# Kernel optimization log

Measured on AMD Instinct MI355X. Metric: run time of the kernel, lower is better.

The kernel has to match this reference:

```python
import jax, jax.numpy as jnp
import numpy as np

DIM = 1024
HEADS = 16
DIM_HEAD = DIM // HEADS

def setup_inputs() -> dict:
    key = jax.random.key(0)
    k1, k2, k3 = jax.random.split(key, 3)
    x = jax.random.normal(k1, (2, 2048, DIM), dtype=jnp.float32)
    # nn.Linear(dim, 3*dim, bias=False): weight [3*dim, dim]; y = x @ W.T
    W_qkv = jax.random.normal(k2, (3 * DIM, DIM), dtype=jnp.float32) * (1.0 / np.sqrt(DIM))
    W_out = jax.random.normal(k3, (DIM, DIM), dtype=jnp.float32) * (1.0 / np.sqrt(DIM))
    return {"x": x, "W_qkv": W_qkv, "W_out": W_out}

def reference(x, W_qkv, W_out):
    b, s, _ = x.shape
    scale = DIM_HEAD ** -0.5
    qkv = x @ W_qkv.T                              # [b, s, 3*dim]
    q, k, v = jnp.split(qkv, 3, axis=-1)
    def to_heads(t):
        return t.reshape(b, s, HEADS, DIM_HEAD).transpose(0, 2, 1, 3)  # [b,h,s,d]
    q, k, v = map(to_heads, (q, k, v))
    scores = jnp.einsum('bhid,bhjd->bhij', q, k) * scale
    causal_mask = jnp.triu(jnp.ones((s, s), dtype=bool), k=1)
    scores = jnp.where(causal_mask, -jnp.inf, scores)
    attn = jax.nn.softmax(scores, axis=-1)
    out = jnp.einsum('bhij,bhjd->bhid', attn, v)
    out = out.transpose(0, 2, 1, 3).reshape(b, s, HEADS * DIM_HEAD)
    return out @ W_out.T
```

## Files before the change

### kernel.cpp

```cpp
#include <hip/hip_runtime.h>
#include <hip/hip_bf16.h>
#include <math.h>

using bf16 = __hip_bfloat16;
typedef __attribute__((ext_vector_type(8))) short bf16x8;
typedef __attribute__((ext_vector_type(4))) short bf16x4;
typedef __attribute__((ext_vector_type(4))) float f32x4;
typedef __attribute__((ext_vector_type(2))) int i32x2;

static __device__ __forceinline__ void gl_lds16(const void* g, void* l) {
  __builtin_amdgcn_global_load_lds(
      (const __attribute__((address_space(1))) unsigned int*)g,
      (__attribute__((address_space(3))) unsigned int*)l, 16, 0, 0);
}

#define MFMA16 __builtin_amdgcn_mfma_f32_16x16x32_bf16
#define MFMA16K16 __builtin_amdgcn_mfma_f32_16x16x16bf16_1k

static __device__ __forceinline__ short f2bf(float f) {
  return (short)((__builtin_bit_cast(unsigned int, f) + 0x8000u) >> 16);
}

__global__ __launch_bounds__(256) void cvt_all(
    const float* __restrict__ x, const float* __restrict__ wqkv,
    const float* __restrict__ wout, bf16* __restrict__ xb,
    bf16* __restrict__ wqkvb, bf16* __restrict__ woutb) {
  const int blk = blockIdx.x;
  const float* src;
  bf16* dst;
  int base;
  if (blk < 4096) {
    src = x; dst = xb; base = blk;
  } else if (blk < 7168) {
    src = wqkv; dst = wqkvb; base = blk - 4096;
  } else {
    src = wout; dst = woutb; base = blk - 7168;
  }
  const int i = (base * 256 + threadIdx.x) * 4;
  const float4 v = *(const float4*)(src + i);
  bf16x4 o;
  o.x = f2bf(v.x);
  o.y = f2bf(v.y);
  o.z = f2bf(v.z);
  o.w = f2bf(v.w);
  *(bf16x4*)(dst + i) = o;
}

template <int K>
static __device__ __forceinline__ void gemm_bt_acc(
    const bf16* __restrict__ A, const bf16* __restrict__ B,
    int rowA0, int rowB0, bf16* As, bf16* Bs, f32x4 acc[4][4]) {
  const int t = threadIdx.x;
  const int w = t >> 6, l = t & 63;
  const int quad = l >> 4, l16 = l & 15;
  const int wm = (w >> 1) * 64, wn = (w & 1) * 64;
  const int c0 = t, c1 = t + 256;
  const bf16* a0 = A + (size_t)(rowA0 + (c0 >> 2)) * K + (c0 & 3) * 8;
  const bf16* a1 = A + (size_t)(rowA0 + (c1 >> 2)) * K + (c1 & 3) * 8;
  const bf16* b0 = B + (size_t)(rowB0 + (c0 >> 2)) * K + (c0 & 3) * 8;
  const bf16* b1 = B + (size_t)(rowB0 + (c1 >> 2)) * K + (c1 & 3) * 8;
  for (int k0 = 0; k0 < K; k0 += 32) {
    __syncthreads();
    gl_lds16(a0 + k0, As + c0 * 8);
    gl_lds16(a1 + k0, As + c1 * 8);
    gl_lds16(b0 + k0, Bs + c0 * 8);
    gl_lds16(b1 + k0, Bs + c1 * 8);
    __syncthreads();
    bf16x8 af[4], bg[4];
#pragma unroll
    for (int i = 0; i < 4; i++)
      af[i] = *(const bf16x8*)(As + (wm + i * 16 + l16) * 32 + quad * 8);
#pragma unroll
    for (int j = 0; j < 4; j++)
      bg[j] = *(const bf16x8*)(Bs + (wn + j * 16 + l16) * 32 + quad * 8);
#pragma unroll
    for (int i = 0; i < 4; i++)
#pragma unroll
      for (int j = 0; j < 4; j++)
        acc[i][j] = MFMA16(af[i], bg[j], acc[i][j], 0, 0, 0);
  }
}

__global__ __launch_bounds__(256) void qkv_gemm(
    const bf16* __restrict__ x, const bf16* __restrict__ Wqkv,
    bf16* __restrict__ Qb, bf16* __restrict__ Kb, bf16* __restrict__ Vt) {
  __shared__ bf16 As[128 * 32];
  __shared__ bf16 Bs[128 * 32];
  f32x4 acc[4][4];
#pragma unroll
  for (int i = 0; i < 4; i++)
#pragma unroll
    for (int j = 0; j < 4; j++) acc[i][j] = (f32x4){0.f, 0.f, 0.f, 0.f};
  const int bm = blockIdx.x, bn = blockIdx.y;
  gemm_bt_acc<1024>(x, Wqkv, bm * 128, bn * 128, As, Bs, acc);

  const int t = threadIdx.x, w = t >> 6, l = t & 63;
  const int quad = l >> 4, l16 = l & 15;
  const int wm = (w >> 1) * 64, wn = (w & 1) * 64;
#pragma unroll
  for (int i = 0; i < 4; i++) {
    const int m0 = bm * 128 + wm + i * 16 + quad * 4;
    const int b = m0 >> 11, s0 = m0 & 2047;
#pragma unroll
    for (int j = 0; j < 4; j++) {
      const int n = bn * 128 + wn + j * 16 + l16;
      const int which = n >> 10;
      const int nn = n & 1023;
      const int h = nn >> 6, d = nn & 63;
      const int bh = b * 16 + h;
      if (which == 2) {
        bf16x4 v4;
#pragma unroll
        for (int r = 0; r < 4; r++)
          v4[r] = (short)__builtin_bit_cast(unsigned short,
                                            __float2bfloat16(acc[i][j][r]));
        *(bf16x4*)(Vt + ((size_t)bh * 64 + d) * 2048 + s0) = v4;
      } else {
        const float sc = (which == 0) ? 0.125f : 1.0f;
        bf16* dst = (which == 0) ? Qb : Kb;
#pragma unroll
        for (int r = 0; r < 4; r++)
          dst[((size_t)bh * 2048 + s0 + r) * 64 + d] =
              __float2bfloat16(acc[i][j][r] * sc);
      }
    }
  }
}

__global__ __launch_bounds__(256) void attn_kernel(
    const bf16* __restrict__ Qb, const bf16* __restrict__ Kb,
    const bf16* __restrict__ Vt, bf16* __restrict__ attn) {
  __shared__ bf16 Qs[64 * 64];
  __shared__ bf16 Ks[128 * 64];
  __shared__ bf16 Vts[64 * 128];
  const int x = blockIdx.x;
  const int bh = x & 31;
  const int idx = x >> 5;
  const int t = threadIdx.x, w = t >> 6, l = t & 63;
  const int quad = l >> 4, l16 = l & 15;
  const bf16x4 ones = {16256, 16256, 16256, 16256};
  const int b = bh >> 4, h = bh & 15;

  for (int pass = 0; pass < 2; pass++) {
    const int qt = pass ? 31 - idx : idx;
    const int q0 = qt * 64;
    if (pass) __syncthreads();

    const bf16* Qg = Qb + ((size_t)bh * 2048 + q0) * 64;
#pragma unroll
    for (int c = t; c < 512; c += 256) {
      const int row = c >> 3, pos = c & 7;
      gl_lds16(Qg + (row * 8 + (pos ^ (row & 7))) * 8, Qs + c * 8);
    }

    f32x4 oacc[4];
    f32x4 lacc = (f32x4){0.f, 0.f, 0.f, 0.f};
#pragma unroll
    for (int md = 0; md < 4; md++) oacc[md] = (f32x4){0.f, 0.f, 0.f, 0.f};

    const int njj = (qt + 2) >> 1;
    for (int jj = 0; jj < njj; jj++) {
      const int j0 = jj * 128;
      __syncthreads();
      const bf16* Kg = Kb + ((size_t)bh * 2048 + j0) * 64;
#pragma unroll
      for (int c = t; c < 1024; c += 256) {
        const int row = c >> 3, pos = c & 7;
        gl_lds16(Kg + (row * 8 + (pos ^ (row & 7))) * 8, Ks + c * 8);
      }
      const bf16* Vg = Vt + (size_t)bh * 64 * 2048 + j0;
#pragma unroll
      for (int c = t; c < 1024; c += 256) {
        const int d = c >> 4, pos = c & 15;
        gl_lds16(Vg + (size_t)d * 2048 + ((pos ^ (d & 15)) * 8), Vts + c * 8);
      }
      __syncthreads();

      f32x4 sacc[8];
#pragma unroll
      for (int mt = 0; mt < 8; mt++) sacc[mt] = (f32x4){0.f, 0.f, 0.f, 0.f};
#pragma unroll
      for (int kk = 0; kk < 2; kk++) {
        const int qrow = w * 16 + l16;
        const int qpos = (kk * 4 + quad) ^ (qrow & 7);
        bf16x8 qf = *(const bf16x8*)(Qs + qrow * 64 + qpos * 8);
#pragma unroll
        for (int mt = 0; mt < 8; mt++) {
          const int row = mt * 16 + l16;
          const int pos = (kk * 4 + quad) ^ (row & 7);
          bf16x8 kf = *(const bf16x8*)(Ks + row * 64 + pos * 8);
          sacc[mt] = MFMA16(kf, qf, sacc[mt], 0, 0, 0);
        }
      }

      bf16x4 pfrag[8];
      if (jj == njj - 1) {
        const int qi = q0 + w * 16 + l16;
#pragma unroll
        for (int mt = 0; mt < 8; mt++) {
          unsigned rb[4];
#pragma unroll
          for (int r = 0; r < 4; r++) {
            const int sg = j0 + mt * 16 + quad * 4 + r;
            const float p = (sg <= qi) ? __expf(sacc[mt][r]) : 0.f;
            rb[r] = __builtin_bit_cast(unsigned, p) + 0x8000u;
          }
          i32x2 pk;
          pk.x = (int)__builtin_amdgcn_perm(rb[1], rb[0], 0x07060302u);
          pk.y = (int)__builtin_amdgcn_perm(rb[3], rb[2], 0x07060302u);
          pfrag[mt] = __builtin_bit_cast(bf16x4, pk);
        }
      } else {
#pragma unroll
        for (int mt = 0; mt < 8; mt++) {
          unsigned rb[4];
#pragma unroll
          for (int r = 0; r < 4; r++) {
            const float p = __expf(sacc[mt][r]);
            rb[r] = __builtin_bit_cast(unsigned, p) + 0x8000u;
          }
          i32x2 pk;
          pk.x = (int)__builtin_amdgcn_perm(rb[1], rb[0], 0x07060302u);
          pk.y = (int)__builtin_amdgcn_perm(rb[3], rb[2], 0x07060302u);
          pfrag[mt] = __builtin_bit_cast(bf16x4, pk);
        }
      }

#pragma unroll
      for (int kt = 0; kt < 8; kt++) {
        lacc = MFMA16K16(ones, pfrag[kt], lacc, 0, 0, 0);
#pragma unroll
        for (int md = 0; md < 4; md++) {
          const int d = md * 16 + l16;
          const int pos = (kt * 2 + (quad >> 1)) ^ (d & 15);
          bf16x4 va =
              *(const bf16x4*)(Vts + d * 128 + pos * 8 + (quad & 1) * 4);
          oacc[md] = MFMA16K16(va, pfrag[kt], oacc[md], 0, 0, 0);
        }
      }
    }

    const float inv = 1.0f / lacc[0];
    const int srow = q0 + w * 16 + l16;
#pragma unroll
    for (int md = 0; md < 4; md++) {
      bf16x4 o4;
#pragma unroll
      for (int r = 0; r < 4; r++) o4[r] = f2bf(oacc[md][r] * inv);
      *(bf16x4*)(attn + ((size_t)b * 2048 + srow) * 1024 + h * 64 + md * 16 +
                 quad * 4) = o4;
    }
  }
}

__global__ __launch_bounds__(256) void out_gemm(
    const bf16* __restrict__ attn, const bf16* __restrict__ Wout,
    float* __restrict__ out) {
  __shared__ bf16 As[128 * 32];
  __shared__ bf16 Bs[64 * 32];
  f32x4 acc[4][2];
#pragma unroll
  for (int i = 0; i < 4; i++)
#pragma unroll
    for (int j = 0; j < 2; j++) acc[i][j] = (f32x4){0.f, 0.f, 0.f, 0.f};
  const int bm = blockIdx.x, bn = blockIdx.y;
  const int t = threadIdx.x, w = t >> 6, l = t & 63;
  const int quad = l >> 4, l16 = l & 15;
  const int wm = (w >> 1) * 64, wn = (w & 1) * 32;
  const int c0 = t, c1 = t + 256;
  const bf16* a0 = attn + (size_t)(bm * 128 + (c0 >> 2)) * 1024 + (c0 & 3) * 8;
  const bf16* a1 = attn + (size_t)(bm * 128 + (c1 >> 2)) * 1024 + (c1 & 3) * 8;
  const bf16* b0 = Wout + (size_t)(bn * 64 + (t >> 2)) * 1024 + (t & 3) * 8;
  for (int k0 = 0; k0 < 1024; k0 += 32) {
    __syncthreads();
    gl_lds16(a0 + k0, As + c0 * 8);
    gl_lds16(a1 + k0, As + c1 * 8);
    gl_lds16(b0 + k0, Bs + t * 8);
    __syncthreads();
    bf16x8 af[4], bg[2];
#pragma unroll
    for (int i = 0; i < 4; i++)
      af[i] = *(const bf16x8*)(As + (wm + i * 16 + l16) * 32 + quad * 8);
#pragma unroll
    for (int j = 0; j < 2; j++)
      bg[j] = *(const bf16x8*)(Bs + (wn + j * 16 + l16) * 32 + quad * 8);
#pragma unroll
    for (int i = 0; i < 4; i++)
#pragma unroll
      for (int j = 0; j < 2; j++)
        acc[i][j] = MFMA16(af[i], bg[j], acc[i][j], 0, 0, 0);
  }
#pragma unroll
  for (int i = 0; i < 4; i++) {
#pragma unroll
    for (int j = 0; j < 2; j++) {
      const int n = bn * 64 + wn + j * 16 + l16;
#pragma unroll
      for (int r = 0; r < 4; r++) {
        const int m = bm * 128 + wm + i * 16 + quad * 4 + r;
        out[(size_t)m * 1024 + n] = acc[i][j][r];
      }
    }
  }
}

extern "C" void kernel_launch(void* const* d_in, const int* in_sizes, int n_in,
                              void* d_out, int out_size, void* d_ws, size_t ws_size,
                              hipStream_t stream) {
  const float* x = (const float*)d_in[0];
  const float* Wqkv = (const float*)d_in[1];
  const float* Wout = (const float*)d_in[2];
  float* out = (float*)d_out;

  char* ws = (char*)d_ws;
  const size_t MB = 1024 * 1024;
  bf16* xb = (bf16*)(ws + 0 * MB);
  bf16* at = (bf16*)(ws + 0 * MB);
  bf16* Wqkvb = (bf16*)(ws + 8 * MB);
  bf16* Woutb = (bf16*)(ws + 14 * MB);
  bf16* Qb = (bf16*)(ws + 16 * MB);
  bf16* Kb = (bf16*)(ws + 24 * MB);
  bf16* Vt = (bf16*)(ws + 32 * MB);

  cvt_all<<<8192, 256, 0, stream>>>(x, Wqkv, Wout, xb, Wqkvb, Woutb);
  qkv_gemm<<<dim3(32, 24), 256, 0, stream>>>(xb, Wqkvb, Qb, Kb, Vt);
  attn_kernel<<<512, 256, 0, stream>>>(Qb, Kb, Vt, at);
  out_gemm<<<dim3(32, 16), 256, 0, stream>>>(at, Woutb, out);
}
```

Before: 166.2 us.

## Double-buffer K/V tiles in attention with async prefetch and MFMA priority

```diff
diff --git a/kernel.cpp b/kernel.cpp
--- a/kernel.cpp
+++ b/kernel.cpp
@@ -131,8 +131,8 @@
     const bf16* __restrict__ Qb, const bf16* __restrict__ Kb,
     const bf16* __restrict__ Vt, bf16* __restrict__ attn) {
   __shared__ bf16 Qs[64 * 64];
-  __shared__ bf16 Ks[128 * 64];
-  __shared__ bf16 Vts[64 * 128];
+  __shared__ bf16 Ks[2][128 * 64];
+  __shared__ bf16 Vts[2][64 * 128];
   const int x = blockIdx.x;
   const int bh = x & 31;
   const int idx = x >> 5;
@@ -141,10 +141,31 @@
   const bf16x4 ones = {16256, 16256, 16256, 16256};
   const int b = bh >> 4, h = bh & 15;
 
+  auto stageKV = [&](int j0, int buf) {
+    const bf16* Kg = Kb + ((size_t)bh * 2048 + j0) * 64;
+    bf16* Ksb = &Ks[buf][0];
+#pragma unroll
+    for (int c = t; c < 1024; c += 256) {
+      const int row = c >> 3, pos = c & 7;
+      gl_lds16(Kg + (row * 8 + (pos ^ (row & 7))) * 8, Ksb + c * 8);
+    }
+    const bf16* Vg = Vt + (size_t)bh * 64 * 2048 + j0;
+    bf16* Vb = &Vts[buf][0];
+#pragma unroll
+    for (int c = t; c < 1024; c += 256) {
+      const int d = c >> 4, pos = c & 15;
+      gl_lds16(Vg + (size_t)d * 2048 + ((pos ^ (d & 15)) * 8), Vb + c * 8);
+    }
+  };
+
   for (int pass = 0; pass < 2; pass++) {
     const int qt = pass ? 31 - idx : idx;
     const int q0 = qt * 64;
-    if (pass) __syncthreads();
+    if (pass) {
+      asm volatile("s_waitcnt lgkmcnt(0)" ::: "memory");
+      __builtin_amdgcn_sched_barrier(0);
+      __builtin_amdgcn_s_barrier();
+    }
 
     const bf16* Qg = Qb + ((size_t)bh * 2048 + q0) * 64;
 #pragma unroll
@@ -152,6 +173,7 @@
       const int row = c >> 3, pos = c & 7;
       gl_lds16(Qg + (row * 8 + (pos ^ (row & 7))) * 8, Qs + c * 8);
     }
+    stageKV(0, 0);
 
     f32x4 oacc[4];
     f32x4 lacc = (f32x4){0.f, 0.f, 0.f, 0.f};
@@ -161,24 +183,27 @@
     const int njj = (qt + 2) >> 1;
     for (int jj = 0; jj < njj; jj++) {
       const int j0 = jj * 128;
-      __syncthreads();
-      const bf16* Kg = Kb + ((size_t)bh * 2048 + j0) * 64;
-#pragma unroll
-      for (int c = t; c < 1024; c += 256) {
-        const int row = c >> 3, pos = c & 7;
-        gl_lds16(Kg + (row * 8 + (pos ^ (row & 7))) * 8, Ks + c * 8);
-      }
-      const bf16* Vg = Vt + (size_t)bh * 64 * 2048 + j0;
-#pragma unroll
-      for (int c = t; c < 1024; c += 256) {
-        const int d = c >> 4, pos = c & 15;
-        gl_lds16(Vg + (size_t)d * 2048 + ((pos ^ (d & 15)) * 8), Vts + c * 8);
-      }
-      __syncthreads();
+      const int cur = jj & 1;
+      asm volatile("s_waitcnt lgkmcnt(0)" ::: "memory");
+      __builtin_amdgcn_sched_barrier(0);
+      __builtin_amdgcn_s_barrier();
+      __builtin_amdgcn_sched_barrier(0);
+      if (jj + 1 < njj) {
+        stageKV(j0 + 128, cur ^ 1);
+        asm volatile("s_waitcnt vmcnt(8)" ::: "memory");
+      } else {
+        asm volatile("s_waitcnt vmcnt(0)" ::: "memory");
+      }
+      __builtin_amdgcn_sched_barrier(0);
+      __builtin_amdgcn_s_barrier();
+      __builtin_amdgcn_sched_barrier(0);
+      const bf16* Ksb = &Ks[cur][0];
+      const bf16* Vb = &Vts[cur][0];
 
       f32x4 sacc[8];
 #pragma unroll
       for (int mt = 0; mt < 8; mt++) sacc[mt] = (f32x4){0.f, 0.f, 0.f, 0.f};
+      __builtin_amdgcn_s_setprio(1);
 #pragma unroll
       for (int kk = 0; kk < 2; kk++) {
         const int qrow = w * 16 + l16;
@@ -188,10 +213,11 @@
         for (int mt = 0; mt < 8; mt++) {
           const int row = mt * 16 + l16;
           const int pos = (kk * 4 + quad) ^ (row & 7);
-          bf16x8 kf = *(const bf16x8*)(Ks + row * 64 + pos * 8);
+          bf16x8 kf = *(const bf16x8*)(Ksb + row * 64 + pos * 8);
           sacc[mt] = MFMA16(kf, qf, sacc[mt], 0, 0, 0);
         }
       }
+      __builtin_amdgcn_s_setprio(0);
 
       bf16x4 pfrag[8];
       if (jj == njj - 1) {
@@ -226,6 +252,7 @@
         }
       }
 
+      __builtin_amdgcn_s_setprio(1);
 #pragma unroll
       for (int kt = 0; kt < 8; kt++) {
         lacc = MFMA16K16(ones, pfrag[kt], lacc, 0, 0, 0);
@@ -234,10 +261,11 @@
           const int d = md * 16 + l16;
           const int pos = (kt * 2 + (quad >> 1)) ^ (d & 15);
           bf16x4 va =
-              *(const bf16x4*)(Vts + d * 128 + pos * 8 + (quad & 1) * 4);
+              *(const bf16x4*)(Vb + d * 128 + pos * 8 + (quad & 1) * 4);
           oacc[md] = MFMA16K16(va, pfrag[kt], oacc[md], 0, 0, 0);
         }
       }
+      __builtin_amdgcn_s_setprio(0);
     }
 
     const float inv = 1.0f / lacc[0];
```

After: 170.5 us. +2.6%, slower.

## Share K/V tile loads between both paired query tiles in attention kernel

Applied to the files above, without the earlier changes.

```diff
diff --git a/kernel.cpp b/kernel.cpp
--- a/kernel.cpp
+++ b/kernel.cpp
@@ -130,116 +130,130 @@
 __global__ __launch_bounds__(256) void attn_kernel(
     const bf16* __restrict__ Qb, const bf16* __restrict__ Kb,
     const bf16* __restrict__ Vt, bf16* __restrict__ attn) {
-  __shared__ bf16 Qs[64 * 64];
+  __shared__ bf16 Qs[2][64 * 64];
   __shared__ bf16 Ks[128 * 64];
   __shared__ bf16 Vts[64 * 128];
   const int x = blockIdx.x;
   const int bh = x & 31;
   const int idx = x >> 5;
+  const int qtA = idx, qtB = 31 - idx;
+  const int q0A = qtA * 64, q0B = qtB * 64;
   const int t = threadIdx.x, w = t >> 6, l = t & 63;
   const int quad = l >> 4, l16 = l & 15;
   const bf16x4 ones = {16256, 16256, 16256, 16256};
   const int b = bh >> 4, h = bh & 15;
 
-  for (int pass = 0; pass < 2; pass++) {
-    const int qt = pass ? 31 - idx : idx;
-    const int q0 = qt * 64;
-    if (pass) __syncthreads();
-
-    const bf16* Qg = Qb + ((size_t)bh * 2048 + q0) * 64;
-#pragma unroll
-    for (int c = t; c < 512; c += 256) {
+  {
+    const bf16* QgA = Qb + ((size_t)bh * 2048 + q0A) * 64;
+    const bf16* QgB = Qb + ((size_t)bh * 2048 + q0B) * 64;
+#pragma unroll
+    for (int c = t; c < 1024; c += 256) {
+      const int tile = c >> 9, cc = c & 511;
+      const int row = cc >> 3, pos = cc & 7;
+      gl_lds16((tile ? QgB : QgA) + (row * 8 + (pos ^ (row & 7))) * 8,
+               &Qs[tile][0] + cc * 8);
+    }
+  }
+
+  f32x4 oaccA[4], oaccB[4];
+  f32x4 laccA = (f32x4){0.f, 0.f, 0.f, 0.f};
+  f32x4 laccB = (f32x4){0.f, 0.f, 0.f, 0.f};
+#pragma unroll
+  for (int md = 0; md < 4; md++) {
+    oaccA[md] = (f32x4){0.f, 0.f, 0.f, 0.f};
+    oaccB[md] = (f32x4){0.f, 0.f, 0.f, 0.f};
+  }
+
+  auto tile_compute = [&](const bf16* Qsb, int q0, bool last, int j0,
+                          f32x4* oacc, f32x4& lacc) {
+    f32x4 sacc[8];
+#pragma unroll
+    for (int mt = 0; mt < 8; mt++) sacc[mt] = (f32x4){0.f, 0.f, 0.f, 0.f};
+#pragma unroll
+    for (int kk = 0; kk < 2; kk++) {
+      const int qrow = w * 16 + l16;
+      const int qpos = (kk * 4 + quad) ^ (qrow & 7);
+      bf16x8 qf = *(const bf16x8*)(Qsb + qrow * 64 + qpos * 8);
+#pragma unroll
+      for (int mt = 0; mt < 8; mt++) {
+        const int row = mt * 16 + l16;
+        const int pos = (kk * 4 + quad) ^ (row & 7);
+        bf16x8 kf = *(const bf16x8*)(Ks + row * 64 + pos * 8);
+        sacc[mt] = MFMA16(kf, qf, sacc[mt], 0, 0, 0);
+      }
+    }
+
+    bf16x4 pfrag[8];
+    if (last) {
+      const int qi = q0 + w * 16 + l16;
+#pragma unroll
+      for (int mt = 0; mt < 8; mt++) {
+        unsigned rb[4];
+#pragma unroll
+        for (int r = 0; r < 4; r++) {
+          const int sg = j0 + mt * 16 + quad * 4 + r;
+          const float p = (sg <= qi) ? __expf(sacc[mt][r]) : 0.f;
+          rb[r] = __builtin_bit_cast(unsigned, p) + 0x8000u;
+        }
+        i32x2 pk;
+        pk.x = (int)__builtin_amdgcn_perm(rb[1], rb[0], 0x07060302u);
+        pk.y = (int)__builtin_amdgcn_perm(rb[3], rb[2], 0x07060302u);
+        pfrag[mt] = __builtin_bit_cast(bf16x4, pk);
+      }
+    } else {
+#pragma unroll
+      for (int mt = 0; mt < 8; mt++) {
+        unsigned rb[4];
+#pragma unroll
+        for (int r = 0; r < 4; r++) {
+          const float p = __expf(sacc[mt][r]);
+          rb[r] = __builtin_bit_cast(unsigned, p) + 0x8000u;
+        }
+        i32x2 pk;
+        pk.x = (int)__builtin_amdgcn_perm(rb[1], rb[0], 0x07060302u);
+        pk.y = (int)__builtin_amdgcn_perm(rb[3], rb[2], 0x07060302u);
+        pfrag[mt] = __builtin_bit_cast(bf16x4, pk);
+      }
+    }
+
+#pragma unroll
+    for (int kt = 0; kt < 8; kt++) {
+      lacc = MFMA16K16(ones, pfrag[kt], lacc, 0, 0, 0);
+#pragma unroll
+      for (int md = 0; md < 4; md++) {
+        const int d = md * 16 + l16;
+        const int pos = (kt * 2 + (quad >> 1)) ^ (d & 15);
+        bf16x4 va = *(const bf16x4*)(Vts + d * 128 + pos * 8 + (quad & 1) * 4);
+        oacc[md] = MFMA16K16(va, pfrag[kt], oacc[md], 0, 0, 0);
+      }
+    }
+  };
+
+  const int njjA = (qtA + 2) >> 1;
+  const int njjB = (qtB + 2) >> 1;
+  for (int jj = 0; jj < njjB; jj++) {
+    const int j0 = jj * 128;
+    __syncthreads();
+    const bf16* Kg = Kb + ((size_t)bh * 2048 + j0) * 64;
+#pragma unroll
+    for (int c = t; c < 1024; c += 256) {
       const int row = c >> 3, pos = c & 7;
-      gl_lds16(Qg + (row * 8 + (pos ^ (row & 7))) * 8, Qs + c * 8);
-    }
-
-    f32x4 oacc[4];
-    f32x4 lacc = (f32x4){0.f, 0.f, 0.f, 0.f};
-#pragma unroll
-    for (int md = 0; md < 4; md++) oacc[md] = (f32x4){0.f, 0.f, 0.f, 0.f};
-
-    const int njj = (qt + 2) >> 1;
-    for (int jj = 0; jj < njj; jj++) {
-      const int j0 = jj * 128;
-      __syncthreads();
-      const bf16* Kg = Kb + ((size_t)bh * 2048 + j0) * 64;
-#pragma unroll
-      for (int c = t; c < 1024; c += 256) {
-        const int row = c >> 3, pos = c & 7;
-        gl_lds16(Kg + (row * 8 + (pos ^ (row & 7))) * 8, Ks + c * 8);
-      }
-      const bf16* Vg = Vt + (size_t)bh * 64 * 2048 + j0;
-#pragma unroll
-      for (int c = t; c < 1024; c += 256) {
-        const int d = c >> 4, pos = c & 15;
-        gl_lds16(Vg + (size_t)d * 2048 + ((pos ^ (d & 15)) * 8), Vts + c * 8);
-      }
-      __syncthreads();
-
-      f32x4 sacc[8];
-#pragma unroll
-      for (int mt = 0; mt < 8; mt++) sacc[mt] = (f32x4){0.f, 0.f, 0.f, 0.f};
-#pragma unroll
-      for (int kk = 0; kk < 2; kk++) {
-        const int qrow = w * 16 + l16;
-        const int qpos = (kk * 4 + quad) ^ (qrow & 7);
-        bf16x8 qf = *(const bf16x8*)(Qs + qrow * 64 + qpos * 8);
-#pragma unroll
-        for (int mt = 0; mt < 8; mt++) {
-          const int row = mt * 16 + l16;
-          const int pos = (kk * 4 + quad) ^ (row & 7);
-          bf16x8 kf = *(const bf16x8*)(Ks + row * 64 + pos * 8);
-          sacc[mt] = MFMA16(kf, qf, sacc[mt], 0, 0, 0);
-        }
-      }
-
-      bf16x4 pfrag[8];
-      if (jj == njj - 1) {
-        const int qi = q0 + w * 16 + l16;
-#pragma unroll
-        for (int mt = 0; mt < 8; mt++) {
-          unsigned rb[4];
-#pragma unroll
-          for (int r = 0; r < 4; r++) {
-            const int sg = j0 + mt * 16 + quad * 4 + r;
-            const float p = (sg <= qi) ? __expf(sacc[mt][r]) : 0.f;
-            rb[r] = __builtin_bit_cast(unsigned, p) + 0x8000u;
-          }
-          i32x2 pk;
-          pk.x = (int)__builtin_amdgcn_perm(rb[1], rb[0], 0x07060302u);
-          pk.y = (int)__builtin_amdgcn_perm(rb[3], rb[2], 0x07060302u);
-          pfrag[mt] = __builtin_bit_cast(bf16x4, pk);
-        }
-      } else {
-#pragma unroll
-        for (int mt = 0; mt < 8; mt++) {
-          unsigned rb[4];
-#pragma unroll
-          for (int r = 0; r < 4; r++) {
-            const float p = __expf(sacc[mt][r]);
-            rb[r] = __builtin_bit_cast(unsigned, p) + 0x8000u;
-          }
-          i32x2 pk;
-          pk.x = (int)__builtin_amdgcn_perm(rb[1], rb[0], 0x07060302u);
-          pk.y = (int)__builtin_amdgcn_perm(rb[3], rb[2], 0x07060302u);
-          pfrag[mt] = __builtin_bit_cast(bf16x4, pk);
-        }
-      }
-
-#pragma unroll
-      for (int kt = 0; kt < 8; kt++) {
-        lacc = MFMA16K16(ones, pfrag[kt], lacc, 0, 0, 0);
-#pragma unroll
-        for (int md = 0; md < 4; md++) {
-          const int d = md * 16 + l16;
-          const int pos = (kt * 2 + (quad >> 1)) ^ (d & 15);
-          bf16x4 va =
-              *(const bf16x4*)(Vts + d * 128 + pos * 8 + (quad & 1) * 4);
-          oacc[md] = MFMA16K16(va, pfrag[kt], oacc[md], 0, 0, 0);
-        }
-      }
-    }
-
+      gl_lds16(Kg + (row * 8 + (pos ^ (row & 7))) * 8, Ks + c * 8);
+    }
+    const bf16* Vg = Vt + (size_t)bh * 64 * 2048 + j0;
+#pragma unroll
+    for (int c = t; c < 1024; c += 256) {
+      const int d = c >> 4, pos = c & 15;
+      gl_lds16(Vg + (size_t)d * 2048 + ((pos ^ (d & 15)) * 8), Vts + c * 8);
+    }
+    __syncthreads();
+
+    if (jj < njjA)
+      tile_compute(&Qs[0][0], q0A, jj == njjA - 1, j0, oaccA, laccA);
+    tile_compute(&Qs[1][0], q0B, jj == njjB - 1, j0, oaccB, laccB);
+  }
+
+  auto epi = [&](const f32x4* oacc, const f32x4& lacc, int q0) {
     const float inv = 1.0f / lacc[0];
     const int srow = q0 + w * 16 + l16;
 #pragma unroll
@@ -250,7 +264,9 @@
       *(bf16x4*)(attn + ((size_t)b * 2048 + srow) * 1024 + h * 64 + md * 16 +
                  quad * 4) = o4;
     }
-  }
+  };
+  epi(oaccA, laccA, q0A);
+  epi(oaccB, laccB, q0B);
 }
 
 __global__ __launch_bounds__(256) void out_gemm(
```

Measured after the change: 169.4 us. Within noise of the previous version (+1.9%).

## Split paired causal query tiles into separate blocks with snake ordering and register Q

Applied to the files above, without the earlier changes.

```diff
diff --git a/kernel.cpp b/kernel.cpp
--- a/kernel.cpp
+++ b/kernel.cpp
@@ -127,129 +127,119 @@
   }
 }
 
-__global__ __launch_bounds__(256) void attn_kernel(
+__global__ __launch_bounds__(256, 4) void attn_kernel(
     const bf16* __restrict__ Qb, const bf16* __restrict__ Kb,
     const bf16* __restrict__ Vt, bf16* __restrict__ attn) {
-  __shared__ bf16 Qs[64 * 64];
   __shared__ bf16 Ks[128 * 64];
   __shared__ bf16 Vts[64 * 128];
   const int x = blockIdx.x;
   const int bh = x & 31;
-  const int idx = x >> 5;
+  const int T = x >> 5;
+  const int s = T >> 3, r = T & 7;
+  const int qt = s * 8 + ((s & 1) ? 7 - r : r);
+  const int q0 = qt * 64;
   const int t = threadIdx.x, w = t >> 6, l = t & 63;
   const int quad = l >> 4, l16 = l & 15;
   const bf16x4 ones = {16256, 16256, 16256, 16256};
   const int b = bh >> 4, h = bh & 15;
 
-  for (int pass = 0; pass < 2; pass++) {
-    const int qt = pass ? 31 - idx : idx;
-    const int q0 = qt * 64;
-    if (pass) __syncthreads();
-
-    const bf16* Qg = Qb + ((size_t)bh * 2048 + q0) * 64;
-#pragma unroll
-    for (int c = t; c < 512; c += 256) {
+  const int qrow = q0 + w * 16 + l16;
+  const bf16* Qg = Qb + ((size_t)bh * 2048 + qrow) * 64 + quad * 8;
+  bf16x8 qreg[2];
+  qreg[0] = *(const bf16x8*)(Qg);
+  qreg[1] = *(const bf16x8*)(Qg + 32);
+
+  f32x4 oacc[4];
+  f32x4 lacc = (f32x4){0.f, 0.f, 0.f, 0.f};
+#pragma unroll
+  for (int md = 0; md < 4; md++) oacc[md] = (f32x4){0.f, 0.f, 0.f, 0.f};
+
+  const int njj = (qt + 2) >> 1;
+  for (int jj = 0; jj < njj; jj++) {
+    const int j0 = jj * 128;
+    __syncthreads();
+    const bf16* Kg = Kb + ((size_t)bh * 2048 + j0) * 64;
+#pragma unroll
+    for (int c = t; c < 1024; c += 256) {
       const int row = c >> 3, pos = c & 7;
-      gl_lds16(Qg + (row * 8 + (pos ^ (row & 7))) * 8, Qs + c * 8);
-    }
-
-    f32x4 oacc[4];
-    f32x4 lacc = (f32x4){0.f, 0.f, 0.f, 0.f};
-#pragma unroll
-    for (int md = 0; md < 4; md++) oacc[md] = (f32x4){0.f, 0.f, 0.f, 0.f};
-
-    const int njj = (qt + 2) >> 1;
-    for (int jj = 0; jj < njj; jj++) {
-      const int j0 = jj * 128;
-      __syncthreads();
-      const bf16* Kg = Kb + ((size_t)bh * 2048 + j0) * 64;
-#pragma unroll
-      for (int c = t; c < 1024; c += 256) {
-        const int row = c >> 3, pos = c & 7;
-        gl_lds16(Kg + (row * 8 + (pos ^ (row & 7))) * 8, Ks + c * 8);
-      }
-      const bf16* Vg = Vt + (size_t)bh * 64 * 2048 + j0;
-#pragma unroll
-      for (int c = t; c < 1024; c += 256) {
-        const int d = c >> 4, pos = c & 15;
-        gl_lds16(Vg + (size_t)d * 2048 + ((pos ^ (d & 15)) * 8), Vts + c * 8);
-      }
-      __syncthreads();
-
-      f32x4 sacc[8];
-#pragma unroll
-      for (int mt = 0; mt < 8; mt++) sacc[mt] = (f32x4){0.f, 0.f, 0.f, 0.f};
-#pragma unroll
-      for (int kk = 0; kk < 2; kk++) {
-        const int qrow = w * 16 + l16;
-        const int qpos = (kk * 4 + quad) ^ (qrow & 7);
-        bf16x8 qf = *(const bf16x8*)(Qs + qrow * 64 + qpos * 8);
-#pragma unroll
-        for (int mt = 0; mt < 8; mt++) {
-          const int row = mt * 16 + l16;
-          const int pos = (kk * 4 + quad) ^ (row & 7);
-          bf16x8 kf = *(const bf16x8*)(Ks + row * 64 + pos * 8);
-          sacc[mt] = MFMA16(kf, qf, sacc[mt], 0, 0, 0);
+      gl_lds16(Kg + (row * 8 + (pos ^ (row & 7))) * 8, Ks + c * 8);
+    }
+    const bf16* Vg = Vt + (size_t)bh * 64 * 2048 + j0;
+#pragma unroll
+    for (int c = t; c < 1024; c += 256) {
+      const int d = c >> 4, pos = c & 15;
+      gl_lds16(Vg + (size_t)d * 2048 + ((pos ^ (d & 15)) * 8), Vts + c * 8);
+    }
+    __syncthreads();
+
+    f32x4 sacc[8];
+#pragma unroll
+    for (int mt = 0; mt < 8; mt++) sacc[mt] = (f32x4){0.f, 0.f, 0.f, 0.f};
+#pragma unroll
+    for (int kk = 0; kk < 2; kk++) {
+#pragma unroll
+      for (int mt = 0; mt < 8; mt++) {
+        const int row = mt * 16 + l16;
+        const int pos = (kk * 4 + quad) ^ (row & 7);
+        bf16x8 kf = *(const bf16x8*)(Ks + row * 64 + pos * 8);
+        sacc[mt] = MFMA16(kf, qreg[kk], sacc[mt], 0, 0, 0);
+      }
+    }
+
+    bf16x4 pfrag[8];
+    if (jj == njj - 1) {
+      const int qi = q0 + w * 16 + l16;
+#pragma unroll
+      for (int mt = 0; mt < 8; mt++) {
+        unsigned rb[4];
+#pragma unroll
+        for (int r2 = 0; r2 < 4; r2++) {
+          const int sg = j0 + mt * 16 + quad * 4 + r2;
+          const float p = (sg <= qi) ? __expf(sacc[mt][r2]) : 0.f;
+          rb[r2] = __builtin_bit_cast(unsigned, p) + 0x8000u;
         }
-      }
-
-      bf16x4 pfrag[8];
-      if (jj == njj - 1) {
-        const int qi = q0 + w * 16 + l16;
-#pragma unroll
-        for (int mt = 0; mt < 8; mt++) {
-          unsigned rb[4];
-#pragma unroll
-          for (int r = 0; r < 4; r++) {
-            const int sg = j0 + mt * 16 + quad * 4 + r;
-            const float p = (sg <= qi) ? __expf(sacc[mt][r]) : 0.f;
-            rb[r] = __builtin_bit_cast(unsigned, p) + 0x8000u;
-          }
-          i32x2 pk;
-          pk.x = (int)__builtin_amdgcn_perm(rb[1], rb[0], 0x07060302u);
-          pk.y = (int)__builtin_amdgcn_perm(rb[3], rb[2], 0x07060302u);
-          pfrag[mt] = __builtin_bit_cast(bf16x4, pk);
+        i32x2 pk;
+        pk.x = (int)__builtin_amdgcn_perm(rb[1], rb[0], 0x07060302u);
+        pk.y = (int)__builtin_amdgcn_perm(rb[3], rb[2], 0x07060302u);
+        pfrag[mt] = __builtin_bit_cast(bf16x4, pk);
+      }
+    } else {
+#pragma unroll
+      for (int mt = 0; mt < 8; mt++) {
+        unsigned rb[4];
+#pragma unroll
+        for (int r2 = 0; r2 < 4; r2++) {
+          const float p = __expf(sacc[mt][r2]);
+          rb[r2] = __builtin_bit_cast(unsigned, p) + 0x8000u;
         }
-      } else {
-#pragma unroll
-        for (int mt = 0; mt < 8; mt++) {
-          unsigned rb[4];
-#pragma unroll
-          for (int r = 0; r < 4; r++) {
-            const float p = __expf(sacc[mt][r]);
-            rb[r] = __builtin_bit_cast(unsigned, p) + 0x8000u;
-          }
-          i32x2 pk;
-          pk.x = (int)__builtin_amdgcn_perm(rb[1], rb[0], 0x07060302u);
-          pk.y = (int)__builtin_amdgcn_perm(rb[3], rb[2], 0x07060302u);
-          pfrag[mt] = __builtin_bit_cast(bf16x4, pk);
-        }
-      }
-
-#pragma unroll
-      for (int kt = 0; kt < 8; kt++) {
-        lacc = MFMA16K16(ones, pfrag[kt], lacc, 0, 0, 0);
-#pragma unroll
-        for (int md = 0; md < 4; md++) {
-          const int d = md * 16 + l16;
-          const int pos = (kt * 2 + (quad >> 1)) ^ (d & 15);
-          bf16x4 va =
-              *(const bf16x4*)(Vts + d * 128 + pos * 8 + (quad & 1) * 4);
-          oacc[md] = MFMA16K16(va, pfrag[kt], oacc[md], 0, 0, 0);
-        }
-      }
-    }
-
-    const float inv = 1.0f / lacc[0];
-    const int srow = q0 + w * 16 + l16;
-#pragma unroll
-    for (int md = 0; md < 4; md++) {
-      bf16x4 o4;
-#pragma unroll
-      for (int r = 0; r < 4; r++) o4[r] = f2bf(oacc[md][r] * inv);
-      *(bf16x4*)(attn + ((size_t)b * 2048 + srow) * 1024 + h * 64 + md * 16 +
-                 quad * 4) = o4;
-    }
+        i32x2 pk;
+        pk.x = (int)__builtin_amdgcn_perm(rb[1], rb[0], 0x07060302u);
+        pk.y = (int)__builtin_amdgcn_perm(rb[3], rb[2], 0x07060302u);
+        pfrag[mt] = __builtin_bit_cast(bf16x4, pk);
+      }
+    }
+
+#pragma unroll
+    for (int kt = 0; kt < 8; kt++) {
+      lacc = MFMA16K16(ones, pfrag[kt], lacc, 0, 0, 0);
+#pragma unroll
+      for (int md = 0; md < 4; md++) {
+        const int d = md * 16 + l16;
+        const int pos = (kt * 2 + (quad >> 1)) ^ (d & 15);
+        bf16x4 va = *(const bf16x4*)(Vts + d * 128 + pos * 8 + (quad & 1) * 4);
+        oacc[md] = MFMA16K16(va, pfrag[kt], oacc[md], 0, 0, 0);
+      }
+    }
+  }
+
+  const float inv = 1.0f / lacc[0];
+#pragma unroll
+  for (int md = 0; md < 4; md++) {
+    bf16x4 o4;
+#pragma unroll
+    for (int r2 = 0; r2 < 4; r2++) o4[r2] = f2bf(oacc[md][r2] * inv);
+    *(bf16x4*)(attn + ((size_t)b * 2048 + qrow) * 1024 + h * 64 + md * 16 +
+               quad * 4) = o4;
   }
 }
 
@@ -324,6 +314,6 @@
 
   cvt_all<<<8192, 256, 0, stream>>>(x, Wqkv, Wout, xb, Wqkvb, Woutb);
   qkv_gemm<<<dim3(32, 24), 256, 0, stream>>>(xb, Wqkvb, Qb, Kb, Vt);
-  attn_kernel<<<512, 256, 0, stream>>>(Qb, Kb, Vt, at);
+  attn_kernel<<<1024, 256, 0, stream>>>(Qb, Kb, Vt, at);
   out_gemm<<<dim3(32, 16), 256, 0, stream>>>(at, Woutb, out);
 }
```

Result: no change. 164.1 us (-1.3%).
